# Optimization experiments

Hardware: AMD Instinct MI355X
Metric: run time of the kernel (lower is better)

Reference implementation:

```python
import jax, jax.numpy as jnp
import numpy as np

CAPACITY = 8_388_608  # 2**23, power of two -> leftmost_leaf == capacity
N_UPDATES = 1_048_576  # 2**20


def setup_inputs() -> dict:
    key = jax.random.key(0)
    k1, k2, k3 = jax.random.split(key, 3)
    # Existing tree buffer; values[1] is root, values[CAPACITY:2*CAPACITY] are leaves.
    tree_values = jax.random.uniform(k1, (2 * CAPACITY,), dtype=jnp.float32)
    # Distinct leaf indices in [0, CAPACITY): torch scatter-assign with duplicate
    # indices is nondeterministic, so the meaningful case is distinct indices.
    indices = jax.random.permutation(k2, CAPACITY)[:N_UPDATES].astype(jnp.int32)
    values = jax.random.uniform(k3, (N_UPDATES,), dtype=jnp.float32)
    return {"tree_values": tree_values, "indices": indices, "values": values}


def reference(tree_values, indices, values):
    """SegmentTree.__setitem__ with op=add: set leaves, propagate sums to root.

    Returns the updated (2*capacity,) tree buffer.
    """
    capacity = tree_values.shape[0] // 2  # static python int
    depth = int(capacity).bit_length() - 1  # log2(capacity) levels to the root
    # _index_to_leaf: with power-of-two capacity, leaf = idx + capacity (no wrap).
    leaf = indices.astype(jnp.int32) + capacity
    tree = tree_values.at[leaf].set(values)
    idx = leaf
    # Original does torch.unique(idx//2) per level purely as an optimization;
    # duplicate parents recompute the identical value, so plain scatter-set of
    # op(left_child, right_child) is the same math and jit-friendly.
    for _ in range(depth):
        idx = idx // 2
        parent = tree[2 * idx] + tree[2 * idx + 1]
        tree = tree.at[idx].set(parent)
    return tree
```

## Files before the change

### kernel.cpp

```cpp
#include <hip/hip_runtime.h>


typedef unsigned int uint;
typedef unsigned char uchar;
typedef unsigned long long ull;

#define NBINS 1024
#define BCAP  2048

__device__ __forceinline__ ull pc64(ull c) {
    ull x = (c | (c >> 1)) & 0x5555555555555555ull;
    x = (x | (x >> 1))  & 0x3333333333333333ull;
    x = (x | (x >> 2))  & 0x0F0F0F0F0F0F0F0Full;
    x = (x | (x >> 4))  & 0x00FF00FF00FF00FFull;
    x = (x | (x >> 8))  & 0x0000FFFF0000FFFFull;
    x = (x | (x >> 16)) & 0x00000000FFFFFFFFull;
    return x;
}

__global__ __launch_bounds__(1024)
void bin_kernel(const int* __restrict__ idx,
                const float* __restrict__ val,
                uint* __restrict__ cnt,
                uint2* __restrict__ bins) {
    __shared__ uint hist[NBINS];
    __shared__ uint rbase[NBINS];
    const int tid = threadIdx.x;
    hist[tid] = 0u;
    __syncthreads();

    const int g = blockIdx.x * 1024 + tid;
    int4   j4 = ((const int4*)idx)[g];
    float4 v4 = ((const float4*)val)[g];
    uint  j[4] = { (uint)j4.x, (uint)j4.y, (uint)j4.z, (uint)j4.w };
    float v[4] = { v4.x, v4.y, v4.z, v4.w };

    #pragma unroll
    for (int e = 0; e < 4; ++e) atomicAdd(&hist[j[e] >> 13], 1u);
    __syncthreads();

    uint h = hist[tid];
    rbase[tid] = h ? atomicAdd(&cnt[tid], h) : 0u;
    hist[tid] = 0u;
    __syncthreads();

    #pragma unroll
    for (int e = 0; e < 4; ++e) {
        uint bin = j[e] >> 13;
        uint r = rbase[bin] + atomicAdd(&hist[bin], 1u);
        if (r < BCAP)
            bins[((size_t)bin << 11) + r] =
                make_uint2(j[e] & 8191u, __float_as_uint(v[e]));
    }
}

__global__ __launch_bounds__(1024)
void merge_kernel(const float* __restrict__ tree,
                  const uint* __restrict__ cnt,
                  const uint2* __restrict__ bins,
                  uint* __restrict__ l13v,
                  uint* __restrict__ l13f,
                  uint* __restrict__ done,
                  float* __restrict__ out, int C) {
    __shared__ float slv[8192];
    __shared__ uchar sfl[8192];
    __shared__ float s9v[16];
    __shared__ uint  s9d[16];
    __shared__ uint  sticket;
    __shared__ float s16v[16];
    __shared__ uint  s16d[16];

    const int b    = blockIdx.x;
    const int tid  = threadIdx.x;
    const int wv   = tid >> 6;
    const int lane = tid & 63;
    const int r    = b * 16 + wv;
    const int leaf0  = tid * 8;
    const int gleaf0 = b * 8192 + leaf0;

    uint c = cnt[b];
    float4 ta = *(const float4*)(tree + C + gleaf0);
    float4 tb = *(const float4*)(tree + C + gleaf0 + 4);
    float4 t1 = *(const float4*)(tree + (C >> 1) + (gleaf0 >> 1));
    float2 t2 = *(const float2*)(tree + (C >> 2) + (gleaf0 >> 2));
    float t3v = tree[(C >> 3) + (gleaf0 >> 3)];
    float pt[6];
    #pragma unroll
    for (int lvl = 4; lvl <= 9; ++lvl) {
        int n = 64 >> (lvl - 3);
        pt[lvl - 4] = tree[(C >> lvl) + (r << (9 - lvl)) + (lane & (n - 1))];
    }
    float pu[4] = {0.f, 0.f, 0.f, 0.f};
    if (wv == 0) {
        #pragma unroll
        for (int lvl = 10; lvl <= 13; ++lvl) {
            int n = 1 << (13 - lvl);
            pu[lvl - 10] =
                tree[(C >> lvl) + (b << (13 - lvl)) + (lane & (n - 1))];
        }
    }

    ((uint2*)sfl)[tid] = make_uint2(0u, 0u);
    __syncthreads();

    if (c > BCAP) c = BCAP;
    const uint2* mybin = bins + ((size_t)b << 11);
    for (uint k = tid; k < c; k += 1024u) {
        uint2 e = mybin[k];
        slv[e.x] = __uint_as_float(e.y);
        sfl[e.x] = 1;
    }
    __syncthreads();

    uint2 fw = *(const uint2*)&sfl[leaf0];
    float4 la = *(const float4*)&slv[leaf0];
    float4 lb = *(const float4*)&slv[leaf0 + 4];

    float l0 = (fw.x & 0x000000FFu) ? la.x : ta.x;
    float l1 = (fw.x & 0x0000FF00u) ? la.y : ta.y;
    float l2 = (fw.x & 0x00FF0000u) ? la.z : ta.z;
    float l3 = (fw.x & 0xFF000000u) ? la.w : ta.w;
    float l4 = (fw.y & 0x000000FFu) ? lb.x : tb.x;
    float l5 = (fw.y & 0x0000FF00u) ? lb.y : tb.y;
    float l6 = (fw.y & 0x00FF0000u) ? lb.z : tb.z;
    float l7 = (fw.y & 0xFF000000u) ? lb.w : tb.w;

    *(float4*)(out + C + gleaf0)     = make_float4(l0, l1, l2, l3);
    *(float4*)(out + C + gleaf0 + 4) = make_float4(l4, l5, l6, l7);

    uint d10 = (fw.x & 0x0000FFFFu) != 0u;
    uint d11 = (fw.x & 0xFFFF0000u) != 0u;
    uint d12 = (fw.y & 0x0000FFFFu) != 0u;
    uint d13 = (fw.y & 0xFFFF0000u) != 0u;
    float4 v1;
    v1.x = d10 ? l0 + l1 : t1.x;
    v1.y = d11 ? l2 + l3 : t1.y;
    v1.z = d12 ? l4 + l5 : t1.z;
    v1.w = d13 ? l6 + l7 : t1.w;
    *(float4*)(out + (C >> 1) + (gleaf0 >> 1)) = v1;

    uint d20 = d10 | d11, d21 = d12 | d13;
    float2 v2;
    v2.x = d20 ? v1.x + v1.y : t2.x;
    v2.y = d21 ? v1.z + v1.w : t2.y;
    *(float2*)(out + (C >> 2) + (gleaf0 >> 2)) = v2;

    uint d3 = d20 | d21;
    float v = d3 ? v2.x + v2.y : t3v;
    out[(C >> 3) + (gleaf0 >> 3)] = v;

    ull m = __ballot(d3 != 0u);
    #pragma unroll
    for (int lvl = 4; lvl <= 9; ++lvl) {
        float a  = __shfl(v, 2 * lane, 64);
        float bb = __shfl(v, 2 * lane + 1, 64);
        m = pc64(m);
        int n = 64 >> (lvl - 3);
        if (lane < n) {
            int node = (C >> lvl) + (r << (9 - lvl)) + lane;
            uint dd = (uint)(m >> lane) & 1u;
            v = dd ? a + bb : pt[lvl - 4];
            out[node] = v;
        }
    }
    if (lane == 0) { s9v[wv] = v; s9d[wv] = (uint)(m & 1ull); }
    __syncthreads();

    if (wv == 0) {
        float vv = lane < 16 ? s9v[lane] : 0.f;
        uint dd  = lane < 16 ? s9d[lane] : 0u;
        ull mm = __ballot(dd != 0u);
        #pragma unroll
        for (int lvl = 10; lvl <= 13; ++lvl) {
            float a  = __shfl(vv, 2 * lane, 64);
            float bb = __shfl(vv, 2 * lane + 1, 64);
            mm = pc64(mm);
            int n = 1 << (13 - lvl);
            if (lane < n) {
                int node = (C >> lvl) + (b << (13 - lvl)) + lane;
                uint d2 = (uint)(mm >> lane) & 1u;
                vv = d2 ? a + bb : pu[lvl - 10];
                out[node] = vv;
            }
        }
        if (lane == 0) {
            uint o1 = atomicExch(&l13v[b], __float_as_uint(vv));
            uint o2 = atomicExch(&l13f[b], (uint)(mm & 1ull));
            asm volatile("" : : "v"(o1), "v"(o2));
            sticket = atomicAdd(done, 1u);
        }
    }
    __syncthreads();
    if (sticket != (uint)gridDim.x - 1u) return;

    {
        const int w2 = tid >> 6;
        float tv = __uint_as_float(atomicOr(&l13v[tid], 0u));
        uint  td = atomicOr(&l13f[tid], 0u);

        ull m2 = __ballot(td != 0u);
        #pragma unroll
        for (int M = 512; M >= 16; M >>= 1) {
            float a  = __shfl(tv, 2 * lane, 64);
            float bb = __shfl(tv, 2 * lane + 1, 64);
            m2 = pc64(m2);
            int nw = M >> 4;
            if (lane < nw) {
                int node = M + nw * w2 + lane;
                uint dd = (uint)(m2 >> lane) & 1u;
                tv = dd ? a + bb : tree[node];
                out[node] = tv;
            }
        }
        if (lane == 0) { s16v[w2] = tv; s16d[w2] = (uint)(m2 & 1ull); }
        __syncthreads();

        if (w2 == 0) {
            float vv2 = lane < 16 ? s16v[lane] : 0.f;
            uint dd2  = lane < 16 ? s16d[lane] : 0u;
            ull mm2 = __ballot(dd2 != 0u);
            #pragma unroll
            for (int M = 8; M >= 1; M >>= 1) {
                float a  = __shfl(vv2, 2 * lane, 64);
                float bb = __shfl(vv2, 2 * lane + 1, 64);
                mm2 = pc64(mm2);
                if (lane < M) {
                    uint d2 = (uint)(mm2 >> lane) & 1u;
                    vv2 = d2 ? a + bb : tree[M + lane];
                    out[M + lane] = vv2;
                }
            }
            if (lane == 0) out[0] = tree[0];
        }
    }
}

extern "C" void kernel_launch(void* const* d_in, const int* in_sizes, int n_in,
                              void* d_out, int out_size, void* d_ws, size_t ws_size,
                              hipStream_t stream) {
    const float* tree    = (const float*)d_in[0];
    const int*   indices = (const int*)d_in[1];
    const float* values  = (const float*)d_in[2];
    float* out = (float*)d_out;

    const int two_cap = in_sizes[0];
    const int C       = two_cap >> 1;
    const int nupd    = in_sizes[1];

    uchar* ws = (uchar*)d_ws;
    uint*  cnt  = (uint*)ws;
    uint*  done = (uint*)(ws + 4096);
    uint*  l13v = (uint*)(ws + 8192);
    uint*  l13f = (uint*)(ws + 12288);
    uint2* bins = (uint2*)(ws + 32768);

    hipMemsetAsync(ws, 0, 4160, stream);
    bin_kernel<<<nupd / 4096, 1024, 0, stream>>>(indices, values, cnt, bins);
    merge_kernel<<<C / 8192, 1024, 0, stream>>>(tree, cnt, bins, l13v, l13f,
                                                done, out, C);
}
```

Baseline: 144.3 us.

## Split merge blocks into quarter-bin 256-thread blocks and widen final reduction

The merge kernel now launches four 256-thread blocks per 8192-leaf bin instead of one 1024-thread block. Each block scans the whole bin but keeps only entries in its quarter, and it reduces up to level 11 rather than 13. The last-arriving block then reduces 4096 partials (16 per thread) through levels 12–15 in registers before the shuffle tree. This is meant to raise occupancy and spread work across more blocks. In exchange each bin's entries are read four times, and the final serial block does more work.

```diff
diff --git a/kernel.cpp b/kernel.cpp
--- a/kernel.cpp
+++ b/kernel.cpp
@@ -54,29 +54,31 @@
     }
 }
 
-__global__ __launch_bounds__(1024)
+__global__ __launch_bounds__(256)
 void merge_kernel(const float* __restrict__ tree,
                   const uint* __restrict__ cnt,
                   const uint2* __restrict__ bins,
-                  uint* __restrict__ l13v,
-                  uint* __restrict__ l13f,
+                  uint* __restrict__ l11v,
+                  uint* __restrict__ l11f,
                   uint* __restrict__ done,
                   float* __restrict__ out, int C) {
-    __shared__ float slv[8192];
-    __shared__ uchar sfl[8192];
-    __shared__ float s9v[16];
-    __shared__ uint  s9d[16];
+    __shared__ float slv[2048];
+    __shared__ uchar sfl[2048];
+    __shared__ float s9v[4];
+    __shared__ uint  s9d[4];
     __shared__ uint  sticket;
     __shared__ float s16v[16];
     __shared__ uint  s16d[16];
 
-    const int b    = blockIdx.x;
+    const int m    = blockIdx.x;
+    const int b    = m >> 2;
+    const uint q   = (uint)(m & 3);
     const int tid  = threadIdx.x;
     const int wv   = tid >> 6;
     const int lane = tid & 63;
-    const int r    = b * 16 + wv;
+    const int r    = m * 4 + wv;
     const int leaf0  = tid * 8;
-    const int gleaf0 = b * 8192 + leaf0;
+    const int gleaf0 = m * 2048 + leaf0;
 
     uint c = cnt[b];
     float4 ta = *(const float4*)(tree + C + gleaf0);
@@ -90,25 +92,28 @@
         int n = 64 >> (lvl - 3);
         pt[lvl - 4] = tree[(C >> lvl) + (r << (9 - lvl)) + (lane & (n - 1))];
     }
-    float pu[4] = {0.f, 0.f, 0.f, 0.f};
+    float pu0 = 0.f, pu1 = 0.f;
     if (wv == 0) {
-        #pragma unroll
-        for (int lvl = 10; lvl <= 13; ++lvl) {
-            int n = 1 << (13 - lvl);
-            pu[lvl - 10] =
-                tree[(C >> lvl) + (b << (13 - lvl)) + (lane & (n - 1))];
-        }
+        pu0 = tree[(C >> 10) + (m << 1) + (lane & 1)];
+        pu1 = tree[(C >> 11) + m];
     }
 
     ((uint2*)sfl)[tid] = make_uint2(0u, 0u);
+    ((float2*)slv)[tid] = make_float2(0.f, 0.f);
+    ((float2*)slv)[tid + 256] = make_float2(0.f, 0.f);
+    ((float2*)slv)[tid + 512] = make_float2(0.f, 0.f);
+    ((float2*)slv)[tid + 768] = make_float2(0.f, 0.f);
     __syncthreads();
 
     if (c > BCAP) c = BCAP;
     const uint2* mybin = bins + ((size_t)b << 11);
-    for (uint k = tid; k < c; k += 1024u) {
+    for (uint k = tid; k < c; k += 256u) {
         uint2 e = mybin[k];
-        slv[e.x] = __uint_as_float(e.y);
-        sfl[e.x] = 1;
+        if ((e.x >> 11) == q) {
+            uint off = e.x & 2047u;
+            slv[off] = __uint_as_float(e.y);
+            sfl[off] = 1;
+        }
     }
     __syncthreads();
 
@@ -149,62 +154,107 @@
     float v = d3 ? v2.x + v2.y : t3v;
     out[(C >> 3) + (gleaf0 >> 3)] = v;
 
-    ull m = __ballot(d3 != 0u);
+    ull mk = __ballot(d3 != 0u);
     #pragma unroll
     for (int lvl = 4; lvl <= 9; ++lvl) {
         float a  = __shfl(v, 2 * lane, 64);
         float bb = __shfl(v, 2 * lane + 1, 64);
-        m = pc64(m);
+        mk = pc64(mk);
         int n = 64 >> (lvl - 3);
         if (lane < n) {
             int node = (C >> lvl) + (r << (9 - lvl)) + lane;
-            uint dd = (uint)(m >> lane) & 1u;
+            uint dd = (uint)(mk >> lane) & 1u;
             v = dd ? a + bb : pt[lvl - 4];
             out[node] = v;
         }
     }
-    if (lane == 0) { s9v[wv] = v; s9d[wv] = (uint)(m & 1ull); }
+    if (lane == 0) { s9v[wv] = v; s9d[wv] = (uint)(mk & 1ull); }
     __syncthreads();
 
     if (wv == 0) {
-        float vv = lane < 16 ? s9v[lane] : 0.f;
-        uint dd  = lane < 16 ? s9d[lane] : 0u;
+        float vv = lane < 4 ? s9v[lane] : 0.f;
+        uint dd  = lane < 4 ? s9d[lane] : 0u;
         ull mm = __ballot(dd != 0u);
-        #pragma unroll
-        for (int lvl = 10; lvl <= 13; ++lvl) {
+        {
             float a  = __shfl(vv, 2 * lane, 64);
             float bb = __shfl(vv, 2 * lane + 1, 64);
             mm = pc64(mm);
-            int n = 1 << (13 - lvl);
-            if (lane < n) {
-                int node = (C >> lvl) + (b << (13 - lvl)) + lane;
+            if (lane < 2) {
                 uint d2 = (uint)(mm >> lane) & 1u;
-                vv = d2 ? a + bb : pu[lvl - 10];
-                out[node] = vv;
+                vv = d2 ? a + bb : pu0;
+                out[(C >> 10) + 2 * m + lane] = vv;
             }
         }
-        if (lane == 0) {
-            uint o1 = atomicExch(&l13v[b], __float_as_uint(vv));
-            uint o2 = atomicExch(&l13f[b], (uint)(mm & 1ull));
-            asm volatile("" : : "v"(o1), "v"(o2));
-            sticket = atomicAdd(done, 1u);
+        {
+            float a  = __shfl(vv, 0, 64);
+            float bb = __shfl(vv, 1, 64);
+            mm = pc64(mm);
+            if (lane == 0) {
+                uint d2 = (uint)mm & 1u;
+                vv = d2 ? a + bb : pu1;
+                out[(C >> 11) + m] = vv;
+                uint o1 = atomicExch(&l11v[m], __float_as_uint(vv));
+                uint o2 = atomicExch(&l11f[m], d2);
+                asm volatile("" : : "v"(o1), "v"(o2));
+                sticket = atomicAdd(done, 1u);
+            }
         }
     }
     __syncthreads();
     if (sticket != (uint)gridDim.x - 1u) return;
 
     {
-        const int w2 = tid >> 6;
-        float tv = __uint_as_float(atomicOr(&l13v[tid], 0u));
-        uint  td = atomicOr(&l13f[tid], 0u);
-
-        ull m2 = __ballot(td != 0u);
+        const int t = tid, w2 = tid >> 6;
+
+        float s11[16]; uint f11[16];
         #pragma unroll
-        for (int M = 512; M >= 16; M >>= 1) {
+        for (int k = 0; k < 16; ++k) {
+            s11[k] = __uint_as_float(atomicOr(&l11v[16 * t + k], 0u));
+            f11[k] = atomicOr(&l11f[16 * t + k], 0u);
+        }
+
+        float4 tA = *(const float4*)(tree + 2048 + 8 * t);
+        float4 tB = *(const float4*)(tree + 2048 + 8 * t + 4);
+        float t12_[8] = { tA.x, tA.y, tA.z, tA.w, tB.x, tB.y, tB.z, tB.w };
+        float v12[8]; uint d12_[8];
+        #pragma unroll
+        for (int k = 0; k < 8; ++k) {
+            uint d = f11[2 * k] | f11[2 * k + 1];
+            d12_[k] = d;
+            v12[k]  = d ? s11[2 * k] + s11[2 * k + 1] : t12_[k];
+        }
+        *(float4*)(out + 2048 + 8 * t)     = make_float4(v12[0], v12[1], v12[2], v12[3]);
+        *(float4*)(out + 2048 + 8 * t + 4) = make_float4(v12[4], v12[5], v12[6], v12[7]);
+
+        float4 t13 = *(const float4*)(tree + 1024 + 4 * t);
+        float t13_[4] = { t13.x, t13.y, t13.z, t13.w };
+        float v13[4]; uint d13_[4];
+        #pragma unroll
+        for (int k = 0; k < 4; ++k) {
+            uint d = d12_[2 * k] | d12_[2 * k + 1];
+            d13_[k] = d;
+            v13[k]  = d ? v12[2 * k] + v12[2 * k + 1] : t13_[k];
+        }
+        *(float4*)(out + 1024 + 4 * t) = make_float4(v13[0], v13[1], v13[2], v13[3]);
+
+        float2 t14 = *(const float2*)(tree + 512 + 2 * t);
+        uint dA = d13_[0] | d13_[1], dB = d13_[2] | d13_[3];
+        float vA = dA ? v13[0] + v13[1] : t14.x;
+        float vB = dB ? v13[2] + v13[3] : t14.y;
+        *(float2*)(out + 512 + 2 * t) = make_float2(vA, vB);
+
+        uint d = dA | dB;
+        float v15 = d ? vA + vB : tree[256 + t];
+        out[256 + t] = v15;
+
+        float tv = v15;
+        ull m2 = __ballot(d != 0u);
+        #pragma unroll
+        for (int M = 128; M >= 16; M >>= 1) {
             float a  = __shfl(tv, 2 * lane, 64);
             float bb = __shfl(tv, 2 * lane + 1, 64);
             m2 = pc64(m2);
-            int nw = M >> 4;
+            int nw = M >> 2;
             if (lane < nw) {
                 int node = M + nw * w2 + lane;
                 uint dd = (uint)(m2 >> lane) & 1u;
@@ -212,22 +262,23 @@
                 out[node] = tv;
             }
         }
-        if (lane == 0) { s16v[w2] = tv; s16d[w2] = (uint)(m2 & 1ull); }
+        if (lane < 4) { s16v[4 * w2 + lane] = tv;
+                        s16d[4 * w2 + lane] = (uint)(m2 >> lane) & 1u; }
         __syncthreads();
 
         if (w2 == 0) {
-            float vv2 = lane < 16 ? s16v[lane] : 0.f;
-            uint dd2  = lane < 16 ? s16d[lane] : 0u;
-            ull mm2 = __ballot(dd2 != 0u);
+            float vv = lane < 16 ? s16v[lane] : 0.f;
+            uint dd  = lane < 16 ? s16d[lane] : 0u;
+            ull mm = __ballot(dd != 0u);
             #pragma unroll
             for (int M = 8; M >= 1; M >>= 1) {
-                float a  = __shfl(vv2, 2 * lane, 64);
-                float bb = __shfl(vv2, 2 * lane + 1, 64);
-                mm2 = pc64(mm2);
+                float a  = __shfl(vv, 2 * lane, 64);
+                float bb = __shfl(vv, 2 * lane + 1, 64);
+                mm = pc64(mm);
                 if (lane < M) {
-                    uint d2 = (uint)(mm2 >> lane) & 1u;
-                    vv2 = d2 ? a + bb : tree[M + lane];
-                    out[M + lane] = vv2;
+                    uint d2 = (uint)(mm >> lane) & 1u;
+                    vv = d2 ? a + bb : tree[M + lane];
+                    out[M + lane] = vv;
                 }
             }
             if (lane == 0) out[0] = tree[0];
@@ -250,12 +301,12 @@
     uchar* ws = (uchar*)d_ws;
     uint*  cnt  = (uint*)ws;
     uint*  done = (uint*)(ws + 4096);
-    uint*  l13v = (uint*)(ws + 8192);
-    uint*  l13f = (uint*)(ws + 12288);
-    uint2* bins = (uint2*)(ws + 32768);
+    uint*  l11v = (uint*)(ws + 8192);
+    uint*  l11f = (uint*)(ws + 24576);
+    uint2* bins = (uint2*)(ws + 65536);
 
     hipMemsetAsync(ws, 0, 4160, stream);
     bin_kernel<<<nupd / 4096, 1024, 0, stream>>>(indices, values, cnt, bins);
-    merge_kernel<<<C / 8192, 1024, 0, stream>>>(tree, cnt, bins, l13v, l13f,
-                                                done, out, C);
+    merge_kernel<<<C / 2048, 256, 0, stream>>>(tree, cnt, bins, l11v, l11f,
+                                               done, out, C);
 }
```

Result: slower. 175.7 us (+21.7%).
